# Kernel tuning notes

Measured on AMD Instinct MI355X. Metric: run time of the kernel, lower is better.

## Reference

```python
import jax, jax.numpy as jnp
import numpy as np

B, L, C = 8, 4096, 256  # batches, points per batch, channels
C8 = C // 8             # query/key projection dim


def setup_inputs() -> dict:
    key = jax.random.key(0)
    ks = jax.random.split(key, 8)
    feats = jax.random.normal(ks[0], (B * L, C), dtype=jnp.float32)
    s_in = 1.0 / np.sqrt(C)
    Wq = jax.random.normal(ks[1], (C8, C), dtype=jnp.float32) * s_in
    bq = jax.random.normal(ks[2], (C8,), dtype=jnp.float32) * 0.01
    Wk = jax.random.normal(ks[3], (C8, C), dtype=jnp.float32) * s_in
    bk = jax.random.normal(ks[4], (C8,), dtype=jnp.float32) * 0.01
    Wv = jax.random.normal(ks[5], (C, C), dtype=jnp.float32) * s_in
    bv = jax.random.normal(ks[6], (C,), dtype=jnp.float32) * 0.01
    # torch init is gamma=0 which zeroes the attention branch; use a nonzero
    # scalar so the attention path contributes to output/gradients.
    gamma = jnp.float32(0.5)
    return {"feats": feats, "Wq": Wq, "bq": bq, "Wk": Wk, "bk": bk,
            "Wv": Wv, "bv": bv, "gamma": gamma,
            "batch_size": B, "points_per_batch": L}


def reference(feats, Wq, bq, Wk, bk, Wv, bv, gamma, batch_size, points_per_batch):
    n, c = feats.shape
    x = feats.reshape(batch_size, points_per_batch, c)  # [B, L, C]
    # conv1d with kernel_size=1 == per-point linear projection
    q = jnp.einsum('blc,dc->bld', x, Wq) + bq  # [B, L, C8]
    k = jnp.einsum('blc,dc->bld', x, Wk) + bk  # [B, L, C8]
    v = jnp.einsum('blc,dc->bld', x, Wv) + bv  # [B, L, C]
    energy = jnp.einsum('bid,bjd->bij', q, k)  # unscaled scores [B, L, L]
    attn = jax.nn.softmax(energy, axis=-1)
    # torch: out[c, l] = sum_j V[c, j] * attn[l, j]  -> [B, C, L]
    out_cl = jnp.einsum('bjc,blj->bcl', v, attn)
    # faithful to torch .view(batch_size, C): raw reshape of [C, L] -> [L, C]
    out = out_cl.reshape(batch_size, points_per_batch, c)
    y = gamma * out + x
    return y.reshape(n, c)
```

## Files before the change

kernel.cpp:

```cpp
#include <hip/hip_runtime.h>

#define LOG2E 1.44269504088896340736f

typedef __attribute__((ext_vector_type(4))) float  f32x4;
typedef __attribute__((ext_vector_type(8))) __bf16 bf16x8;
typedef __attribute__((ext_vector_type(4))) __bf16 bf16x4;

static __device__ __forceinline__ f32x4 mfma16(bf16x8 a, bf16x8 b, f32x4 c) {
  return __builtin_amdgcn_mfma_f32_16x16x32_bf16(a, b, c, 0, 0, 0);
}


__global__ void cvt_f32_to_bf16(const float* __restrict__ s, __bf16* __restrict__ d, int n4) {
  const int stride = gridDim.x * blockDim.x;
  for (int i = blockIdx.x * blockDim.x + threadIdx.x; i < n4; i += stride) {
    const float4 v = reinterpret_cast<const float4*>(s)[i];
    bf16x4 o = { (__bf16)v.x, (__bf16)v.y, (__bf16)v.z, (__bf16)v.w };
    reinterpret_cast<bf16x4*>(d)[i] = o;
  }
}

__global__ __launch_bounds__(256) void qk_proj(
    const __bf16* __restrict__ x, const __bf16* __restrict__ wq, const __bf16* __restrict__ wk,
    const float* __restrict__ bq, const float* __restrict__ bk,
    __bf16* __restrict__ Qh, __bf16* __restrict__ Ql,
    __bf16* __restrict__ Kh, __bf16* __restrict__ Kl)
{
  const int w = threadIdx.x >> 6, lane = threadIdx.x & 63;
  const int lo = lane & 15, hi = lane >> 4;
  const int m0 = blockIdx.x * 64 + w * 16;
  f32x4 acc[4] = {};
  for (int ks = 0; ks < 8; ++ks) {
    const bf16x8 a = *reinterpret_cast<const bf16x8*>(x + (size_t)(m0 + lo) * 256 + ks * 32 + hi * 8);
    #pragma unroll
    for (int nt = 0; nt < 4; ++nt) {
      const int d = nt * 16 + lo;
      const __bf16* wrow = (nt < 2) ? (wq + d * 256) : (wk + (d - 32) * 256);
      const bf16x8 bfr = *reinterpret_cast<const bf16x8*>(wrow + ks * 32 + hi * 8);
      acc[nt] = mfma16(a, bfr, acc[nt]);
    }
  }
  #pragma unroll
  for (int nt = 0; nt < 4; ++nt) {
    const int d = nt * 16 + lo;
    const float bias = (nt < 2) ? bq[d] : bk[d - 32];
    #pragma unroll
    for (int r = 0; r < 4; ++r) {
      const size_t row = m0 + hi * 4 + r;
      float v = acc[nt][r] + bias;
      if (nt < 2) v *= LOG2E;
      const __bf16 vh = (__bf16)v;
      const __bf16 vl = (__bf16)(v - (float)vh);
      if (nt < 2) { Qh[row * 32 + d] = vh;        Ql[row * 32 + d] = vl; }
      else        { Kh[row * 32 + (d - 32)] = vh; Kl[row * 32 + (d - 32)] = vl; }
    }
  }
}

__global__ __launch_bounds__(256) void v_proj(
    const __bf16* __restrict__ x, const __bf16* __restrict__ wv, const float* __restrict__ bv,
    __bf16* __restrict__ VT)
{
  const int w = threadIdx.x >> 6, lane = threadIdx.x & 63;
  const int lo = lane & 15, hi = lane >> 4;
  const int bn = blockIdx.x & 511, bc = blockIdx.x >> 9;
  const int n0 = bn * 64;
  const int c0 = bc * 64 + w * 16;
  f32x4 acc[4] = {};
  for (int ks = 0; ks < 8; ++ks) {
    const bf16x8 a = *reinterpret_cast<const bf16x8*>(wv + (size_t)(c0 + lo) * 256 + ks * 32 + hi * 8);
    #pragma unroll
    for (int nt = 0; nt < 4; ++nt) {
      const bf16x8 bfr = *reinterpret_cast<const bf16x8*>(x + (size_t)(n0 + nt * 16 + lo) * 256 + ks * 32 + hi * 8);
      acc[nt] = mfma16(a, bfr, acc[nt]);
    }
  }
  const int bb = n0 >> 12;
  #pragma unroll
  for (int nt = 0; nt < 4; ++nt) {
    const int nl = n0 + nt * 16 + lo;
    #pragma unroll
    for (int r = 0; r < 4; ++r) {
      const int c = c0 + hi * 4 + r;
      VT[(size_t)(bb * 256 + c) * 4096 + (nl & 4095)] = (__bf16)(acc[nt][r] + bv[c]);
    }
  }
}

__global__ __launch_bounds__(256, 2) void attn_kernel(
    const __bf16* __restrict__ Qhi, const __bf16* __restrict__ Qlo,
    const __bf16* __restrict__ Khi, const __bf16* __restrict__ Klo,
    const __bf16* __restrict__ VT,
    const float* __restrict__ feats, const float* __restrict__ gptr,
    float* __restrict__ out)
{
  __shared__ alignas(16) __bf16 vt[256 * 64];
  __shared__ alignas(16) __bf16 plds[4 * 16 * 64];
  const int tid  = threadIdx.x;
  const int w    = tid >> 6, lane = tid & 63;
  const int lo   = lane & 15, hi = lane >> 4;
  const int b    = blockIdx.x & 7;
  const int qt   = blockIdx.x >> 3;
  const int qbase = qt * 64 + w * 16;

  const size_t qrow = (size_t)(b * 4096 + qbase + lo) * 32 + hi * 8;
  const bf16x8 qh = *reinterpret_cast<const bf16x8*>(Qhi + qrow);
  const bf16x8 ql = *reinterpret_cast<const bf16x8*>(Qlo + qrow);

  const __bf16* vbase = VT + (size_t)b * 256 * 4096;
  char* vtb = (char*)vt;
  char* plb = (char*)(plds + w * 1024);

  const int sc0  = w * 64 + (lane >> 3);
  const int jblk = lane & 7;

  f32x4 o[16] = {};
  float lacc[4] = {0.f, 0.f, 0.f, 0.f};

  bf16x8 stg[8];
  #pragma unroll
  for (int i = 0; i < 8; ++i)
    stg[i] = *reinterpret_cast<const bf16x8*>(vbase + (size_t)(sc0 + i * 8) * 4096 + jblk * 8);
  bf16x8 kh[4], kl[4];
  #pragma unroll
  for (int jt = 0; jt < 4; ++jt) {
    const size_t krow = (size_t)(b * 4096 + jt * 16 + lo) * 32 + hi * 8;
    kh[jt] = *reinterpret_cast<const bf16x8*>(Khi + krow);
    kl[jt] = *reinterpret_cast<const bf16x8*>(Klo + krow);
  }

  for (int jb = 0; jb < 4096; jb += 64) {
    #pragma unroll
    for (int i = 0; i < 8; ++i) {
      const int c = sc0 + i * 8;
      *reinterpret_cast<bf16x8*>(vtb + c * 128 + ((jblk ^ (c & 7)) << 4)) = stg[i];
    }
    __syncthreads();

    f32x4 s[4];
    #pragma unroll
    for (int jt = 0; jt < 4; ++jt) {
      f32x4 acc = {0.f, 0.f, 0.f, 0.f};
      acc = mfma16(qh, kh[jt], acc);
      acc = mfma16(qh, kl[jt], acc);
      acc = mfma16(ql, kh[jt], acc);
      s[jt] = acc;
    }

    const int jn = (jb + 64) & 4095;
    bf16x8 stg2[8];
    #pragma unroll
    for (int i = 0; i < 8; ++i)
      stg2[i] = *reinterpret_cast<const bf16x8*>(vbase + (size_t)(sc0 + i * 8) * 4096 + jn + jblk * 8);
    bf16x8 kh2[4], kl2[4];
    #pragma unroll
    for (int jt = 0; jt < 4; ++jt) {
      const size_t krow = (size_t)(b * 4096 + jn + jt * 16 + lo) * 32 + hi * 8;
      kh2[jt] = *reinterpret_cast<const bf16x8*>(Khi + krow);
      kl2[jt] = *reinterpret_cast<const bf16x8*>(Klo + krow);
    }

    float p[4][4];
    #pragma unroll
    for (int jt = 0; jt < 4; ++jt) {
      #pragma unroll
      for (int r = 0; r < 4; ++r) {
        const float pv = __builtin_amdgcn_exp2f(s[jt][r]);
        p[jt][r] = pv;
        lacc[r] += pv;
      }
    }

    #pragma unroll
    for (int jt = 0; jt < 4; ++jt) {
      #pragma unroll
      for (int r = 0; r < 4; ++r) {
        const int q = hi * 4 + r;
        const int off = q * 128 + (((jt * 32 + ((lo & 8) << 1)) ^ ((q & 7) << 4)) | ((lo & 7) * 2));
        *reinterpret_cast<__bf16*>(plb + off) = (__bf16)p[jt][r];
      }
    }
    bf16x8 pf[2];
    #pragma unroll
    for (int ks = 0; ks < 2; ++ks)
      pf[ks] = *reinterpret_cast<const bf16x8*>(plb + lo * 128 + ((ks * 64 + hi * 16) ^ ((lo & 7) << 4)));

    __builtin_amdgcn_s_setprio(1);
    #pragma unroll
    for (int ks = 0; ks < 2; ++ks) {
      #pragma unroll
      for (int ct = 0; ct < 16; ++ct) {
        const int c = ct * 16 + lo;
        const bf16x8 vf = *reinterpret_cast<const bf16x8*>(vtb + c * 128 + (((ks * 4 + hi) ^ (c & 7)) << 4));
        o[ct] = mfma16(pf[ks], vf, o[ct]);
      }
    }
    __builtin_amdgcn_s_setprio(0);
    __syncthreads();

    #pragma unroll
    for (int i = 0; i < 8; ++i) stg[i] = stg2[i];
    #pragma unroll
    for (int jt = 0; jt < 4; ++jt) { kh[jt] = kh2[jt]; kl[jt] = kl2[jt]; }
  }

  const float g = gptr[0];
  float inv[4];
  #pragma unroll
  for (int r = 0; r < 4; ++r) {
    float t = lacc[r];
    t += __shfl_xor(t, 1);
    t += __shfl_xor(t, 2);
    t += __shfl_xor(t, 4);
    t += __shfl_xor(t, 8);
    inv[r] = g / t;
  }
  const size_t obase = (size_t)b * (256 * 4096);
  const int q_lo = qbase + hi * 4;
  #pragma unroll
  for (int ct = 0; ct < 16; ++ct) {
    const int c = ct * 16 + lo;
    const size_t idx = obase + (size_t)c * 4096 + q_lo;
    const float4 xr = *reinterpret_cast<const float4*>(feats + idx);
    float4 y;
    y.x = o[ct][0] * inv[0] + xr.x;
    y.y = o[ct][1] * inv[1] + xr.y;
    y.z = o[ct][2] * inv[2] + xr.z;
    y.w = o[ct][3] * inv[3] + xr.w;
    *reinterpret_cast<float4*>(out + idx) = y;
  }
}

extern "C" void kernel_launch(void* const* d_in, const int* in_sizes, int n_in,
                              void* d_out, int out_size, void* d_ws, size_t ws_size,
                              hipStream_t stream) {
  const float* feats = (const float*)d_in[0];
  const float* Wq    = (const float*)d_in[1];
  const float* bq    = (const float*)d_in[2];
  const float* Wk    = (const float*)d_in[3];
  const float* bk    = (const float*)d_in[4];
  const float* Wv    = (const float*)d_in[5];
  const float* bv    = (const float*)d_in[6];
  const float* gamma = (const float*)d_in[7];
  float* out = (float*)d_out;

  char* ws = (char*)d_ws;
  const size_t SZ_X  = 16777216;
  const size_t SZ_QK = 2097152;
  const size_t SZ_VT = 16777216;
  const size_t NEED = SZ_X + 4 * SZ_QK + SZ_VT + 2 * 16384 + 131072;
  if (ws_size < NEED) return;

  __bf16* xb  = (__bf16*)(ws);
  __bf16* Qh  = (__bf16*)(ws + SZ_X);
  __bf16* Ql  = (__bf16*)(ws + SZ_X + SZ_QK);
  __bf16* Kh  = (__bf16*)(ws + SZ_X + 2 * SZ_QK);
  __bf16* Kl  = (__bf16*)(ws + SZ_X + 3 * SZ_QK);
  __bf16* VT  = (__bf16*)(ws + SZ_X + 4 * SZ_QK);
  __bf16* wqb = (__bf16*)(ws + SZ_X + 4 * SZ_QK + SZ_VT);
  __bf16* wkb = wqb + 32 * 256;
  __bf16* wvb = wkb + 32 * 256;

  cvt_f32_to_bf16<<<2048, 256, 0, stream>>>(feats, xb, 8388608 / 4);
  cvt_f32_to_bf16<<<8,    256, 0, stream>>>(Wq, wqb, 8192 / 4);
  cvt_f32_to_bf16<<<8,    256, 0, stream>>>(Wk, wkb, 8192 / 4);
  cvt_f32_to_bf16<<<64,   256, 0, stream>>>(Wv, wvb, 65536 / 4);

  qk_proj<<<512, 256, 0, stream>>>(xb, wqb, wkb, bq, bk, Qh, Ql, Kh, Kl);
  v_proj <<<2048, 256, 0, stream>>>(xb, wvb, bv, VT);
  attn_kernel<<<512, 256, 0, stream>>>(Qh, Ql, Kh, Kl, VT, feats, gamma, out);
}
```

Measured before the change: 195.7 us.

## Split PV output by channel across waves and share P via double-buffered LDS

Each wave now owns 64 output channels for all 64 queries of the block and loads its V fragments straight from global memory into registers, instead of staging the full 256x64 V tile through LDS. The S=QK^T MFMAs swap operand order so P lands transposed. P is written with packed bf16x4 stores into a double-buffered shared tile so all waves can read every query row, leaving one barrier per iteration. Row sums are reduced through a small LDS array at the end. This removes V LDS staging and its swizzled reads, at the cost of more global V traffic per wave and cross-wave dependence on P.

```diff
diff --git a/kernel.cpp b/kernel.cpp
--- a/kernel.cpp
+++ b/kernel.cpp
@@ -94,140 +94,135 @@
     const float* __restrict__ feats, const float* __restrict__ gptr,
     float* __restrict__ out)
 {
-  __shared__ alignas(16) __bf16 vt[256 * 64];
-  __shared__ alignas(16) __bf16 plds[4 * 16 * 64];
+  __shared__ alignas(16) __bf16 pbuf0[64 * 64];
+  __shared__ alignas(16) __bf16 pbuf1[64 * 64];
+  __shared__ float lred[64];
+
   const int tid  = threadIdx.x;
   const int w    = tid >> 6, lane = tid & 63;
   const int lo   = lane & 15, hi = lane >> 4;
   const int b    = blockIdx.x & 7;
   const int qt   = blockIdx.x >> 3;
-  const int qbase = qt * 64 + w * 16;
-
-  const size_t qrow = (size_t)(b * 4096 + qbase + lo) * 32 + hi * 8;
+  const int qblk = qt * 64;
+  const int qw   = qblk + w * 16;
+  const int cw   = w * 64;
+
+  const size_t qrow = (size_t)(b * 4096 + qw + lo) * 32 + hi * 8;
   const bf16x8 qh = *reinterpret_cast<const bf16x8*>(Qhi + qrow);
   const bf16x8 ql = *reinterpret_cast<const bf16x8*>(Qlo + qrow);
 
   const __bf16* vbase = VT + (size_t)b * 256 * 4096;
-  char* vtb = (char*)vt;
-  char* plb = (char*)(plds + w * 1024);
-
-  const int sc0  = w * 64 + (lane >> 3);
-  const int jblk = lane & 7;
-
-  f32x4 o[16] = {};
-  float lacc[4] = {0.f, 0.f, 0.f, 0.f};
-
-  bf16x8 stg[8];
-  #pragma unroll
-  for (int i = 0; i < 8; ++i)
-    stg[i] = *reinterpret_cast<const bf16x8*>(vbase + (size_t)(sc0 + i * 8) * 4096 + jblk * 8);
+  const __bf16* khp[4];
+  const __bf16* klp[4];
+  #pragma unroll
+  for (int jt = 0; jt < 4; ++jt) {
+    const size_t off = (size_t)(b * 4096 + jt * 16 + lo) * 32 + hi * 8;
+    khp[jt] = Khi + off;
+    klp[jt] = Klo + off;
+  }
+  const __bf16* vp[4];
+  #pragma unroll
+  for (int ct = 0; ct < 4; ++ct)
+    vp[ct] = vbase + (size_t)(cw + ct * 16 + lo) * 4096 + hi * 8;
+
+  char* const pb0 = (char*)pbuf0;
+  char* const pb1 = (char*)pbuf1;
+  const int swz  = (lo & 7) << 4;
+  const int pwr  = (w * 16 + lo) * 128;
+
+  f32x4 o[4][4] = {};
+  f32x4 lacc4 = {0.f, 0.f, 0.f, 0.f};
+
   bf16x8 kh[4], kl[4];
   #pragma unroll
-  for (int jt = 0; jt < 4; ++jt) {
-    const size_t krow = (size_t)(b * 4096 + jt * 16 + lo) * 32 + hi * 8;
-    kh[jt] = *reinterpret_cast<const bf16x8*>(Khi + krow);
-    kl[jt] = *reinterpret_cast<const bf16x8*>(Klo + krow);
-  }
-
-  for (int jb = 0; jb < 4096; jb += 64) {
-    #pragma unroll
-    for (int i = 0; i < 8; ++i) {
-      const int c = sc0 + i * 8;
-      *reinterpret_cast<bf16x8*>(vtb + c * 128 + ((jblk ^ (c & 7)) << 4)) = stg[i];
-    }
-    __syncthreads();
+  for (int jt = 0; jt < 4; ++jt) { kh[jt] = *reinterpret_cast<const bf16x8*>(khp[jt]);
+                                   kl[jt] = *reinterpret_cast<const bf16x8*>(klp[jt]); }
+
+  for (int t = 0; t < 64; ++t) {
+    const int jb = t * 64;
+    bf16x8 vf[8];
+    #pragma unroll
+    for (int ks = 0; ks < 2; ++ks)
+      #pragma unroll
+      for (int ct = 0; ct < 4; ++ct)
+        vf[ks * 4 + ct] = *reinterpret_cast<const bf16x8*>(vp[ct] + jb + ks * 32);
 
     f32x4 s[4];
     #pragma unroll
     for (int jt = 0; jt < 4; ++jt) {
       f32x4 acc = {0.f, 0.f, 0.f, 0.f};
-      acc = mfma16(qh, kh[jt], acc);
-      acc = mfma16(qh, kl[jt], acc);
-      acc = mfma16(ql, kh[jt], acc);
+      acc = mfma16(kh[jt], qh, acc);
+      acc = mfma16(kl[jt], qh, acc);
+      acc = mfma16(kh[jt], ql, acc);
       s[jt] = acc;
     }
 
     const int jn = (jb + 64) & 4095;
-    bf16x8 stg2[8];
-    #pragma unroll
-    for (int i = 0; i < 8; ++i)
-      stg2[i] = *reinterpret_cast<const bf16x8*>(vbase + (size_t)(sc0 + i * 8) * 4096 + jn + jblk * 8);
     bf16x8 kh2[4], kl2[4];
     #pragma unroll
     for (int jt = 0; jt < 4; ++jt) {
-      const size_t krow = (size_t)(b * 4096 + jn + jt * 16 + lo) * 32 + hi * 8;
-      kh2[jt] = *reinterpret_cast<const bf16x8*>(Khi + krow);
-      kl2[jt] = *reinterpret_cast<const bf16x8*>(Klo + krow);
-    }
-
-    float p[4][4];
+      kh2[jt] = *reinterpret_cast<const bf16x8*>(khp[jt] + (size_t)jn * 32);
+      kl2[jt] = *reinterpret_cast<const bf16x8*>(klp[jt] + (size_t)jn * 32);
+    }
+
+    char* const pw = ((t & 1) ? pb1 : pb0) + pwr;
     #pragma unroll
     for (int jt = 0; jt < 4; ++jt) {
-      #pragma unroll
-      for (int r = 0; r < 4; ++r) {
-        const float pv = __builtin_amdgcn_exp2f(s[jt][r]);
-        p[jt][r] = pv;
-        lacc[r] += pv;
-      }
-    }
-
-    #pragma unroll
-    for (int jt = 0; jt < 4; ++jt) {
-      #pragma unroll
-      for (int r = 0; r < 4; ++r) {
-        const int q = hi * 4 + r;
-        const int off = q * 128 + (((jt * 32 + ((lo & 8) << 1)) ^ ((q & 7) << 4)) | ((lo & 7) * 2));
-        *reinterpret_cast<__bf16*>(plb + off) = (__bf16)p[jt][r];
-      }
-    }
-    bf16x8 pf[2];
-    #pragma unroll
-    for (int ks = 0; ks < 2; ++ks)
-      pf[ks] = *reinterpret_cast<const bf16x8*>(plb + lo * 128 + ((ks * 64 + hi * 16) ^ ((lo & 7) << 4)));
-
+      f32x4 p4;
+      #pragma unroll
+      for (int r = 0; r < 4; ++r) p4[r] = __builtin_amdgcn_exp2f(s[jt][r]);
+      lacc4 += p4;
+      bf16x4 pk = { (__bf16)p4[0], (__bf16)p4[1], (__bf16)p4[2], (__bf16)p4[3] };
+      *reinterpret_cast<bf16x4*>(pw + ((jt * 32 + hi * 8) ^ swz)) = pk;
+    }
+    __syncthreads();
+
+    const char* const pr = (t & 1) ? pb1 : pb0;
     __builtin_amdgcn_s_setprio(1);
     #pragma unroll
     for (int ks = 0; ks < 2; ++ks) {
-      #pragma unroll
-      for (int ct = 0; ct < 16; ++ct) {
-        const int c = ct * 16 + lo;
-        const bf16x8 vf = *reinterpret_cast<const bf16x8*>(vtb + c * 128 + (((ks * 4 + hi) ^ (c & 7)) << 4));
-        o[ct] = mfma16(pf[ks], vf, o[ct]);
-      }
+      bf16x8 pf[4];
+      #pragma unroll
+      for (int qt2 = 0; qt2 < 4; ++qt2)
+        pf[qt2] = *reinterpret_cast<const bf16x8*>(pr + (qt2 * 16 + lo) * 128 + ((ks * 64 + hi * 16) ^ swz));
+      #pragma unroll
+      for (int qt2 = 0; qt2 < 4; ++qt2)
+        #pragma unroll
+        for (int ct = 0; ct < 4; ++ct)
+          o[qt2][ct] = mfma16(pf[qt2], vf[ks * 4 + ct], o[qt2][ct]);
     }
     __builtin_amdgcn_s_setprio(0);
-    __syncthreads();
-
-    #pragma unroll
-    for (int i = 0; i < 8; ++i) stg[i] = stg2[i];
+
     #pragma unroll
     for (int jt = 0; jt < 4; ++jt) { kh[jt] = kh2[jt]; kl[jt] = kl2[jt]; }
   }
 
+  float lacc = lacc4[0] + lacc4[1] + lacc4[2] + lacc4[3];
+  lacc += __shfl_xor(lacc, 16);
+  lacc += __shfl_xor(lacc, 32);
+  if (lane < 16) lred[w * 16 + lo] = lacc;
+  __syncthreads();
+
   const float g = gptr[0];
-  float inv[4];
-  #pragma unroll
-  for (int r = 0; r < 4; ++r) {
-    float t = lacc[r];
-    t += __shfl_xor(t, 1);
-    t += __shfl_xor(t, 2);
-    t += __shfl_xor(t, 4);
-    t += __shfl_xor(t, 8);
-    inv[r] = g / t;
-  }
   const size_t obase = (size_t)b * (256 * 4096);
-  const int q_lo = qbase + hi * 4;
-  #pragma unroll
-  for (int ct = 0; ct < 16; ++ct) {
-    const int c = ct * 16 + lo;
-    const size_t idx = obase + (size_t)c * 4096 + q_lo;
-    const float4 xr = *reinterpret_cast<const float4*>(feats + idx);
-    float4 y;
-    y.x = o[ct][0] * inv[0] + xr.x;
-    y.y = o[ct][1] * inv[1] + xr.y;
-    y.z = o[ct][2] * inv[2] + xr.z;
-    y.w = o[ct][3] * inv[3] + xr.w;
-    *reinterpret_cast<float4*>(out + idx) = y;
+  #pragma unroll
+  for (int qt2 = 0; qt2 < 4; ++qt2) {
+    float inv[4];
+    #pragma unroll
+    for (int r = 0; r < 4; ++r) inv[r] = g / lred[qt2 * 16 + hi * 4 + r];
+    const int q_lo = qblk + qt2 * 16 + hi * 4;
+    #pragma unroll
+    for (int ct = 0; ct < 4; ++ct) {
+      const int c = cw + ct * 16 + lo;
+      const size_t idx = obase + (size_t)c * 4096 + q_lo;
+      const float4 xr = *reinterpret_cast<const float4*>(feats + idx);
+      float4 y;
+      y.x = o[qt2][ct][0] * inv[0] + xr.x;
+      y.y = o[qt2][ct][1] * inv[1] + xr.y;
+      y.z = o[qt2][ct][2] * inv[2] + xr.z;
+      y.w = o[qt2][ct][3] * inv[3] + xr.w;
+      *reinterpret_cast<float4*>(out + idx) = y;
+    }
   }
 }
 
```

Measured after the change: 248.3 us. 26.9% more time.
